# Kernel tuning notes

Measured on AMD Instinct MI355X. Metric: run time of the kernel, lower is better.

## Reference

```python
import jax, jax.numpy as jnp
import numpy as np

NUM_CLASSES = 21
THRESH = 0.5
NEGPOS = 3
VAR0, VAR1 = 0.1, 0.2
FEAT = 19
N_ANCH = 9
B = 256
NUM_OBJS = 12
P = FEAT * FEAT * N_ANCH  # 3249


def make_priors():
    # 19x19 grid, 3 scales x 3 aspect ratios (1, 2, 1/2) -> 9 anchors/cell, center form
    cxy = (np.arange(FEAT, dtype=np.float32) + 0.5) / FEAT
    cx, cy = np.meshgrid(cxy, cxy, indexing='ij')  # [19,19]
    scales = np.array([0.1, 0.2, 0.35], dtype=np.float32)
    ratios = np.array([1.0, 2.0, 0.5], dtype=np.float32)
    w = (scales[:, None] * np.sqrt(ratios)[None, :]).reshape(-1)  # [9]
    h = (scales[:, None] / np.sqrt(ratios)[None, :]).reshape(-1)
    cx = np.broadcast_to(cx[:, :, None], (FEAT, FEAT, N_ANCH))
    cy = np.broadcast_to(cy[:, :, None], (FEAT, FEAT, N_ANCH))
    w = np.broadcast_to(w[None, None, :], (FEAT, FEAT, N_ANCH))
    h = np.broadcast_to(h[None, None, :], (FEAT, FEAT, N_ANCH))
    pri = np.stack([cx, cy, w, h], axis=-1).reshape(-1, 4)
    return jnp.asarray(np.clip(pri, 1e-3, 1.0))


def setup_inputs() -> dict:
    key = jax.random.key(0)
    k1, k2, k3, k4, k5 = jax.random.split(key, 5)
    loc_data = jax.random.normal(k1, (B, P, 4), dtype=jnp.float32)
    conf_data = jax.random.normal(k2, (B, P, NUM_CLASSES), dtype=jnp.float32)
    priors = make_priors()
    xy = jax.random.uniform(k3, (B, NUM_OBJS, 2), minval=0.05, maxval=0.65)
    wh = jax.random.uniform(k4, (B, NUM_OBJS, 2), minval=0.05, maxval=0.30)
    labels = jax.random.randint(k5, (B, NUM_OBJS), 0, NUM_CLASSES - 1).astype(jnp.float32)
    targets = jnp.concatenate([xy, xy + wh, labels[..., None]], axis=-1)  # [B,O,5]
    return {"loc_data": loc_data, "conf_data": conf_data, "priors": priors, "targets": targets}


def point_form(boxes):  # (cx,cy,w,h) -> (x1,y1,x2,y2)
    return jnp.concatenate([boxes[:, :2] - boxes[:, 2:] / 2,
                            boxes[:, :2] + boxes[:, 2:] / 2], axis=1)


def jaccard(a, b):  # a: [n,4], b: [m,4] point form -> [n,m]
    lt = jnp.maximum(a[:, None, :2], b[None, :, :2])
    rb = jnp.minimum(a[:, None, 2:], b[None, :, 2:])
    inter = jnp.prod(jnp.clip(rb - lt, 0.0, None), axis=-1)
    area_a = jnp.prod(a[:, 2:] - a[:, :2], axis=-1)
    area_b = jnp.prod(b[:, 2:] - b[:, :2], axis=-1)
    return inter / (area_a[:, None] + area_b[None, :] - inter)


def encode(matched, priors):  # matched point-form [P,4], priors center-form [P,4]
    g_cxcy = ((matched[:, :2] + matched[:, 2:]) / 2 - priors[:, :2]) / (VAR0 * priors[:, 2:])
    g_wh = jnp.log((matched[:, 2:] - matched[:, :2]) / priors[:, 2:]) / VAR1
    return jnp.concatenate([g_cxcy, g_wh], axis=1)


def match_one(truths, labels, priors, priors_pt):
    overlaps = jaccard(truths, priors_pt)          # [O,P]
    best_prior_idx = jnp.argmax(overlaps, axis=1)  # [O]
    best_truth_ov = jnp.max(overlaps, axis=0)      # [P]
    best_truth_idx = jnp.argmax(overlaps, axis=0)  # [P]
    best_truth_ov = best_truth_ov.at[best_prior_idx].set(2.0)
    best_truth_idx = best_truth_idx.at[best_prior_idx].set(jnp.arange(truths.shape[0]))
    matches = truths[best_truth_idx]               # [P,4]
    conf = labels[best_truth_idx] + 1
    conf = jnp.where(best_truth_ov < THRESH, 0, conf)
    return encode(matches, priors), conf


def reference(loc_data, conf_data, priors, targets):
    truths = targets[:, :, :4]
    labels = targets[:, :, 4].astype(jnp.int32)
    priors_pt = point_form(priors)
    loc_t, conf_t = jax.vmap(lambda t, l: match_one(t, l, priors, priors_pt))(truths, labels)
    loc_t = jax.lax.stop_gradient(loc_t)
    conf_t = jax.lax.stop_gradient(conf_t)

    pos = conf_t > 0                                               # [B,P]
    # smooth L1 (sum) over matched priors
    d = loc_data - loc_t
    ad = jnp.abs(d)
    sl1 = jnp.where(ad < 1.0, 0.5 * d * d, ad - 0.5)
    loss_l = jnp.sum(sl1 * pos[..., None].astype(sl1.dtype))

    # per-prior CE = logsumexp - logit[target]
    lse = jax.nn.logsumexp(conf_data, axis=-1)                     # [B,P]
    gathered = jnp.take_along_axis(conf_data, conf_t[..., None], axis=2)[..., 0]
    ce = lse - gathered                                            # [B,P]

    # hard negative mining: double argsort rank of neg losses
    loss_c_mine = jnp.where(pos, 0.0, ce)
    loss_idx = jnp.argsort(-loss_c_mine, axis=1)
    idx_rank = jnp.argsort(loss_idx, axis=1)
    num_pos = jnp.sum(pos, axis=1, keepdims=True)                  # [B,1]
    num_neg = jnp.minimum(NEGPOS * num_pos, P - 1)
    neg = idx_rank < num_neg

    sel = pos | neg
    loss_c = jnp.sum(jnp.where(sel, ce, 0.0))

    have_centerloss = jnp.max(sel.reshape(B, FEAT, FEAT, N_ANCH), axis=3).reshape(-1)
    conf_t_featuremap = jnp.max(conf_t.reshape(B, FEAT, FEAT, N_ANCH), axis=3).reshape(-1)

    N = jnp.sum(num_pos).astype(loc_data.dtype)
    return loss_l / N, loss_c / N, conf_t_featuremap, have_centerloss
```

## Files before the change

### kernel.cpp

```cpp
#include <hip/hip_runtime.h>
#include <math.h>

#pragma clang fp contract(off)

#define BB      256
#define PP      3249
#define NCLS    21
#define NOBJ    12
#define CELLS   361
#define THRESH_ 0.5f
#define NPB     13


__global__ __launch_bounds__(256) void k1_lse_iou(
    const float* __restrict__ conf, const float* __restrict__ priors,
    const float* __restrict__ targets,
    float* __restrict__ g_lse, float* __restrict__ g_bov,
    unsigned char* __restrict__ g_bidx, unsigned long long* __restrict__ g_best)
{
    const int b = blockIdx.y;
    const int tid = threadIdx.x, lane = tid & 63;
    const int p = blockIdx.x * 256 + tid;
    const bool valid = (p < PP);

    __shared__ float s_tx1[NOBJ], s_ty1[NOBJ], s_tx2[NOBJ], s_ty2[NOBJ];
    __shared__ float s_area_t[NOBJ];
    if (tid < NOBJ) {
        const float* t = targets + ((size_t)b * NOBJ + tid) * 5;
        float x1 = t[0], y1 = t[1], x2 = t[2], y2 = t[3];
        s_tx1[tid] = x1; s_ty1[tid] = y1; s_tx2[tid] = x2; s_ty2[tid] = y2;
        s_area_t[tid] = (x2 - x1) * (y2 - y1);
    }
    __syncthreads();

    float iou_j[NOBJ];
    float bov = -1.0f; int bidx = 0;
    if (valid) {
        float cx = priors[4*p+0], cy = priors[4*p+1], w = priors[4*p+2], h = priors[4*p+3];
        float px1 = cx - w / 2.0f, py1 = cy - h / 2.0f;
        float px2 = cx + w / 2.0f, py2 = cy + h / 2.0f;
        float area_p = (px2 - px1) * (py2 - py1);
#pragma unroll
        for (int j = 0; j < NOBJ; ++j) {
            float ltx = fmaxf(s_tx1[j], px1);
            float lty = fmaxf(s_ty1[j], py1);
            float rbx = fminf(s_tx2[j], px2);
            float rby = fminf(s_ty2[j], py2);
            float iw = fmaxf(rbx - ltx, 0.0f);
            float ih = fmaxf(rby - lty, 0.0f);
            float inter = iw * ih;
            float iou = inter / ((s_area_t[j] + area_p) - inter);
            iou_j[j] = iou;
            if (iou > bov) { bov = iou; bidx = j; }
        }
    } else {
#pragma unroll
        for (int j = 0; j < NOBJ; ++j) iou_j[j] = -1.0f;
    }

#pragma unroll
    for (int j = 0; j < NOBJ; ++j) {
        float ov = iou_j[j]; int ix = valid ? p : 0x7FFFFFFF;
#pragma unroll
        for (int off = 32; off > 0; off >>= 1) {
            float ov2 = __shfl_xor(ov, off);
            int   ix2 = __shfl_xor(ix, off);
            if (ov2 > ov || (ov2 == ov && ix2 < ix)) { ov = ov2; ix = ix2; }
        }
        if (lane == 0 && ov >= 0.0f) {
            unsigned long long key =
                ((unsigned long long)__float_as_uint(ov) << 32)
                | (unsigned int)(0xFFFFFFFFu - (unsigned int)ix);
            atomicMax(&g_best[b * NOBJ + j], key);
        }
    }

    if (valid) {
        const size_t bp = (size_t)b * PP + p;
        g_bov[bp] = bov;
        g_bidx[bp] = (unsigned char)bidx;

        const float* cd = conf + bp * NCLS;
        float m = cd[0];
#pragma unroll
        for (int k = 1; k < NCLS; ++k) m = fmaxf(m, cd[k]);
        float s = 0.0f;
#pragma unroll
        for (int k = 0; k < NCLS; ++k) s += expf(cd[k] - m);
        g_lse[bp] = logf(s) + m;
    }
}

__global__ __launch_bounds__(1024) void k2_select(
    const float* __restrict__ loc, const float* __restrict__ conf,
    const float* __restrict__ priors, const float* __restrict__ targets,
    const float* __restrict__ g_lse, const float* __restrict__ g_bov,
    const unsigned char* __restrict__ g_bidx, const unsigned long long* __restrict__ g_best,
    int* __restrict__ numpos, double* __restrict__ lossl,
    double* __restrict__ lossc, float* __restrict__ out)
{
    const int b = blockIdx.x, tid = threadIdx.x;
    const int lane = tid & 63, wid = tid >> 6;

    __shared__ float s_tx1[NOBJ], s_ty1[NOBJ], s_tx2[NOBJ], s_ty2[NOBJ];
    __shared__ int   s_label[NOBJ];
    __shared__ int   s_bpi[NOBJ];
    __shared__ unsigned long long s_key[PP];
    __shared__ float s_ce[PP];
    __shared__ unsigned char s_ct[PP];
    __shared__ unsigned char s_sel[PP];
    __shared__ int s_hist[256];
    __shared__ int s_chosen, s_knext, s_nneg;
    __shared__ double s_pl[16];
    __shared__ int    s_pn[16];
    __shared__ double s_pc[16];

    if (tid < NOBJ) {
        const float* t = targets + ((size_t)b * NOBJ + tid) * 5;
        s_tx1[tid] = t[0]; s_ty1[tid] = t[1]; s_tx2[tid] = t[2]; s_ty2[tid] = t[3];
        s_label[tid] = (int)t[4];
        s_bpi[tid] = (int)(0xFFFFFFFFu - (unsigned int)(g_best[b * NOBJ + tid] & 0xFFFFFFFFull));
    }
    __syncthreads();

    int my_pos = 0;
    double my_lossl = 0.0;
    const float* confb = conf + (size_t)b * PP * NCLS;
    for (int p = tid; p < PP; p += 1024) {
        const size_t bp = (size_t)b * PP + p;
        int jov = -1;
#pragma unroll
        for (int j = 0; j < NOBJ; ++j) if (s_bpi[j] == p) jov = j;
        int idx; float ov;
        if (jov >= 0) { idx = jov; ov = 2.0f; }
        else          { idx = (int)g_bidx[bp]; ov = g_bov[bp]; }
        int c = (ov < THRESH_) ? 0 : (s_label[idx] + 1);
        s_ct[p] = (unsigned char)c;

        float ce = g_lse[bp] - confb[(size_t)p * NCLS + c];
        s_ce[p] = ce;
        float v = (c > 0) ? 0.0f : ce;
        s_key[p] = ((unsigned long long)__float_as_uint(v) << 32)
                 | (unsigned int)(0xFFFFFFFFu - (unsigned int)p);

        if (c > 0) {
            ++my_pos;
            float cx = priors[4*p+0], cy = priors[4*p+1], w = priors[4*p+2], h = priors[4*p+3];
            float m0 = s_tx1[idx], m1 = s_ty1[idx], m2 = s_tx2[idx], m3 = s_ty2[idx];
            float g0 = ((m0 + m2) / 2.0f - cx) / (0.1f * w);
            float g1 = ((m1 + m3) / 2.0f - cy) / (0.1f * h);
            float g2 = logf((m2 - m0) / w) / 0.2f;
            float g3 = logf((m3 - m1) / h) / 0.2f;
            const float* ld = loc + (bp) * 4;
            float d0 = ld[0] - g0, d1 = ld[1] - g1, d2 = ld[2] - g2, d3 = ld[3] - g3;
            float a0 = fabsf(d0), a1 = fabsf(d1), a2 = fabsf(d2), a3 = fabsf(d3);
            my_lossl += (double)((a0 < 1.0f) ? 0.5f * d0 * d0 : a0 - 0.5f);
            my_lossl += (double)((a1 < 1.0f) ? 0.5f * d1 * d1 : a1 - 0.5f);
            my_lossl += (double)((a2 < 1.0f) ? 0.5f * d2 * d2 : a2 - 0.5f);
            my_lossl += (double)((a3 < 1.0f) ? 0.5f * d3 * d3 : a3 - 0.5f);
        }
    }
#pragma unroll
    for (int off = 32; off > 0; off >>= 1) {
        my_lossl += __shfl_down(my_lossl, off);
        my_pos   += __shfl_down(my_pos, off);
    }
    if (lane == 0) { s_pl[wid] = my_lossl; s_pn[wid] = my_pos; }
    __syncthreads();
    if (tid == 0) {
        double L = 0.0; int n = 0;
#pragma unroll
        for (int w2 = 0; w2 < 16; ++w2) { L += s_pl[w2]; n += s_pn[w2]; }
        lossl[b] = L; numpos[b] = n;
        s_nneg = min(3 * n, PP - 1);
    }
    __syncthreads();

    unsigned long long prefix = 0ull, pmask = 0ull;
    int kk = s_nneg;
    for (int d = 56; d >= 0; d -= 8) {
        if (tid < 256) s_hist[tid] = 0;
        __syncthreads();
        for (int i = tid; i < PP; i += 1024) {
            unsigned long long key = s_key[i];
            if ((key & pmask) == prefix)
                atomicAdd(&s_hist[(int)((key >> d) & 0xFF)], 1);
        }
        __syncthreads();
        if (tid < 64) {
            int h0 = s_hist[4*lane+0], h1 = s_hist[4*lane+1];
            int h2 = s_hist[4*lane+2], h3 = s_hist[4*lane+3];
            int ls = h0 + h1 + h2 + h3;
            int x = ls;
#pragma unroll
            for (int off = 1; off < 64; off <<= 1) {
                int y = __shfl_down(x, off);
                if (lane + off < 64) x += y;
            }
            int excl = x - ls;
            int cb3 = excl;
            int cb2 = cb3 + h3;
            int cb1 = cb2 + h2;
            int cb0 = cb1 + h1;
            if (cb3 < kk && kk <= cb3 + h3) { s_chosen = 4*lane+3; s_knext = kk - cb3; }
            if (cb2 < kk && kk <= cb2 + h2) { s_chosen = 4*lane+2; s_knext = kk - cb2; }
            if (cb1 < kk && kk <= cb1 + h1) { s_chosen = 4*lane+1; s_knext = kk - cb1; }
            if (cb0 < kk && kk <= cb0 + h0) { s_chosen = 4*lane+0; s_knext = kk - cb0; }
        }
        __syncthreads();
        prefix |= ((unsigned long long)(unsigned int)s_chosen) << d;
        pmask  |= 0xFFull << d;
        kk = s_knext;
        __syncthreads();
    }
    const unsigned long long kth = prefix;

    double my_c = 0.0;
    for (int p = tid; p < PP; p += 1024) {
        int c = s_ct[p];
        bool sel = (c > 0) || (s_key[p] >= kth);
        s_sel[p] = sel ? 1 : 0;
        if (sel) my_c += (double)s_ce[p];
    }
    __syncthreads();

    for (int cI = tid; cI < CELLS; cI += 1024) {
        int mc = 0, hv = 0;
#pragma unroll
        for (int a = 0; a < 9; ++a) {
            int p = cI * 9 + a;
            int cv = s_ct[p];
            mc = (cv > mc) ? cv : mc;
            hv |= s_sel[p];
        }
        out[2 + (size_t)b * CELLS + cI] = (float)mc;
        out[2 + (size_t)BB * CELLS + (size_t)b * CELLS + cI] = (float)hv;
    }

#pragma unroll
    for (int off = 32; off > 0; off >>= 1) my_c += __shfl_down(my_c, off);
    if (lane == 0) s_pc[wid] = my_c;
    __syncthreads();
    if (tid == 0) {
        double L = 0.0;
#pragma unroll
        for (int w2 = 0; w2 < 16; ++w2) L += s_pc[w2];
        lossc[b] = L;
    }
}

__global__ __launch_bounds__(256) void finalize_kernel(
    const int* __restrict__ numpos, const double* __restrict__ lossl,
    const double* __restrict__ lossc, float* __restrict__ out)
{
    __shared__ double s_l[256], s_c[256];
    __shared__ int s_n[256];
    int tid = threadIdx.x;
    s_n[tid] = numpos[tid];
    s_l[tid] = lossl[tid];
    s_c[tid] = lossc[tid];
    __syncthreads();
    for (int s = 128; s > 0; s >>= 1) {
        if (tid < s) { s_n[tid] += s_n[tid + s]; s_l[tid] += s_l[tid + s]; s_c[tid] += s_c[tid + s]; }
        __syncthreads();
    }
    if (tid == 0) {
        double N = (double)s_n[0];
        out[0] = (float)(s_l[0] / N);
        out[1] = (float)(s_c[0] / N);
    }
}

extern "C" void kernel_launch(void* const* d_in, const int* in_sizes, int n_in,
                              void* d_out, int out_size, void* d_ws, size_t ws_size,
                              hipStream_t stream) {
    const float* loc     = (const float*)d_in[0];
    const float* conf    = (const float*)d_in[1];
    const float* priors  = (const float*)d_in[2];
    const float* targets = (const float*)d_in[3];
    float* out = (float*)d_out;

    double* ws_lossl  = (double*)d_ws;
    double* ws_lossc  = ws_lossl + BB;
    unsigned long long* ws_best = (unsigned long long*)(ws_lossc + BB);
    int*    ws_numpos = (int*)(ws_best + (size_t)BB * NOBJ);
    float*  ws_lse    = (float*)(ws_numpos + BB);
    float*  ws_bov    = ws_lse + (size_t)BB * PP;
    unsigned char* ws_bidx = (unsigned char*)(ws_bov + (size_t)BB * PP);

    hipMemsetAsync(ws_best, 0, (size_t)BB * NOBJ * sizeof(unsigned long long), stream);

    hipLaunchKernelGGL(k1_lse_iou, dim3(NPB, BB), dim3(256), 0, stream,
                       conf, priors, targets, ws_lse, ws_bov, ws_bidx, ws_best);
    hipLaunchKernelGGL(k2_select, dim3(BB), dim3(1024), 0, stream,
                       loc, conf, priors, targets, ws_lse, ws_bov, ws_bidx, ws_best,
                       ws_numpos, ws_lossl, ws_lossc, out);
    hipLaunchKernelGGL(finalize_kernel, dim3(1), dim3(256), 0, stream,
                       ws_numpos, ws_lossl, ws_lossc, out);
}
```

Measured before the change: 157.3 us.

## Split matching from CE, stage conf in LDS coalesced, skip radix passes on index bits

Moves IoU matching into a small kernel that writes one packed byte per prior (threshold flag plus best index). A new flat kernel stages each 256-row block of conf into shared memory with float4 loads, computes logsumexp and CE, and writes the sort key and class per prior. It also accumulates positives, loc loss and positive CE with global atomics, so k2 no longer rereads conf, loc and priors. The radix select skips two middle byte passes by fixing those index bits. This cuts redundant global traffic and uncoalesced conf reads, at the cost of an extra launch, per-prior double atomics, and a shortcut in the selection that relies on the key layout.

```diff
diff --git a/kernel.cpp b/kernel.cpp
--- a/kernel.cpp
+++ b/kernel.cpp
@@ -10,21 +10,19 @@
 #define CELLS   361
 #define THRESH_ 0.5f
 #define NPB     13
-
-
-__global__ __launch_bounds__(256) void k1_lse_iou(
-    const float* __restrict__ conf, const float* __restrict__ priors,
-    const float* __restrict__ targets,
-    float* __restrict__ g_lse, float* __restrict__ g_bov,
-    unsigned char* __restrict__ g_bidx, unsigned long long* __restrict__ g_best)
+#define NROWBLK 3249
+
+
+__global__ __launch_bounds__(256) void k0_match(
+    const float* __restrict__ priors, const float* __restrict__ targets,
+    unsigned char* __restrict__ g_mi, unsigned long long* __restrict__ g_best)
 {
     const int b = blockIdx.y;
     const int tid = threadIdx.x, lane = tid & 63;
     const int p = blockIdx.x * 256 + tid;
     const bool valid = (p < PP);
 
-    __shared__ float s_tx1[NOBJ], s_ty1[NOBJ], s_tx2[NOBJ], s_ty2[NOBJ];
-    __shared__ float s_area_t[NOBJ];
+    __shared__ float s_tx1[NOBJ], s_ty1[NOBJ], s_tx2[NOBJ], s_ty2[NOBJ], s_area_t[NOBJ];
     if (tid < NOBJ) {
         const float* t = targets + ((size_t)b * NOBJ + tid) * 5;
         float x1 = t[0], y1 = t[1], x2 = t[2], y2 = t[3];
@@ -53,6 +51,8 @@
             iou_j[j] = iou;
             if (iou > bov) { bov = iou; bidx = j; }
         }
+        g_mi[(size_t)b * PP + p] =
+            (unsigned char)(((bov < THRESH_) ? 0 : 0x80) | bidx);
     } else {
 #pragma unroll
         for (int j = 0; j < NOBJ; ++j) iou_j[j] = -1.0f;
@@ -74,111 +74,109 @@
             atomicMax(&g_best[b * NOBJ + j], key);
         }
     }
-
-    if (valid) {
-        const size_t bp = (size_t)b * PP + p;
-        g_bov[bp] = bov;
-        g_bidx[bp] = (unsigned char)bidx;
-
-        const float* cd = conf + bp * NCLS;
-        float m = cd[0];
-#pragma unroll
-        for (int k = 1; k < NCLS; ++k) m = fmaxf(m, cd[k]);
-        float s = 0.0f;
-#pragma unroll
-        for (int k = 0; k < NCLS; ++k) s += expf(cd[k] - m);
-        g_lse[bp] = logf(s) + m;
+}
+
+__global__ __launch_bounds__(256) void k1_ce(
+    const float* __restrict__ conf, const float* __restrict__ loc,
+    const float* __restrict__ priors, const float* __restrict__ targets,
+    const unsigned char* __restrict__ g_mi, const unsigned long long* __restrict__ g_best,
+    unsigned long long* __restrict__ g_key, unsigned char* __restrict__ g_ct,
+    int* __restrict__ numpos, double* __restrict__ lossl, double* __restrict__ lossc)
+{
+    __shared__ float s_conf[256 * NCLS];
+    const int tid = threadIdx.x;
+    const size_t row0 = (size_t)blockIdx.x * 256;
+
+    const float4* src = (const float4*)(conf + row0 * NCLS);
+    float4* dst = (float4*)s_conf;
+#pragma unroll
+    for (int i = tid; i < 1344; i += 256) dst[i] = src[i];
+    __syncthreads();
+
+    const size_t r = row0 + tid;
+    const int b = (int)(r / PP);
+    const int p = (int)(r - (size_t)b * PP);
+
+    int jov = -1;
+#pragma unroll
+    for (int j = 0; j < NOBJ; ++j) {
+        unsigned long long k = g_best[b * NOBJ + j];
+        int bp = (int)(0xFFFFFFFFu - (unsigned int)(k & 0xFFFFFFFFull));
+        if (bp == p) jov = j;
+    }
+    const unsigned char mi = g_mi[r];
+    int idx, c;
+    if (jov >= 0) {
+        idx = jov;
+        c = (int)targets[((size_t)b * NOBJ + idx) * 5 + 4] + 1;
+    } else {
+        idx = mi & 15;
+        c = (mi & 0x80) ? ((int)targets[((size_t)b * NOBJ + idx) * 5 + 4] + 1) : 0;
+    }
+    g_ct[r] = (unsigned char)c;
+
+    const float* cd = s_conf + tid * NCLS;
+    float m = cd[0];
+#pragma unroll
+    for (int k = 1; k < NCLS; ++k) m = fmaxf(m, cd[k]);
+    float s = 0.0f;
+#pragma unroll
+    for (int k = 0; k < NCLS; ++k) s += expf(cd[k] - m);
+    float ce = (logf(s) + m) - cd[c];
+
+    float v = (c > 0) ? 0.0f : ce;
+    g_key[r] = ((unsigned long long)__float_as_uint(v) << 32)
+             | (unsigned int)(0xFFFFFFFFu - (unsigned int)p);
+
+    if (c > 0) {
+        atomicAdd(&numpos[b], 1);
+        atomicAdd(&lossc[b], (double)ce);
+        const float* t = targets + ((size_t)b * NOBJ + idx) * 5;
+        float m0 = t[0], m1 = t[1], m2 = t[2], m3 = t[3];
+        float cx = priors[4*p+0], cy = priors[4*p+1], w = priors[4*p+2], h = priors[4*p+3];
+        float g0 = ((m0 + m2) / 2.0f - cx) / (0.1f * w);
+        float g1 = ((m1 + m3) / 2.0f - cy) / (0.1f * h);
+        float g2 = logf((m2 - m0) / w) / 0.2f;
+        float g3 = logf((m3 - m1) / h) / 0.2f;
+        const float* ld = loc + r * 4;
+        float d0 = ld[0] - g0, d1 = ld[1] - g1, d2 = ld[2] - g2, d3 = ld[3] - g3;
+        float a0 = fabsf(d0), a1 = fabsf(d1), a2 = fabsf(d2), a3 = fabsf(d3);
+        double sl = (double)((a0 < 1.0f) ? 0.5f * d0 * d0 : a0 - 0.5f)
+                  + (double)((a1 < 1.0f) ? 0.5f * d1 * d1 : a1 - 0.5f)
+                  + (double)((a2 < 1.0f) ? 0.5f * d2 * d2 : a2 - 0.5f)
+                  + (double)((a3 < 1.0f) ? 0.5f * d3 * d3 : a3 - 0.5f);
+        atomicAdd(&lossl[b], sl);
     }
 }
 
 __global__ __launch_bounds__(1024) void k2_select(
-    const float* __restrict__ loc, const float* __restrict__ conf,
-    const float* __restrict__ priors, const float* __restrict__ targets,
-    const float* __restrict__ g_lse, const float* __restrict__ g_bov,
-    const unsigned char* __restrict__ g_bidx, const unsigned long long* __restrict__ g_best,
-    int* __restrict__ numpos, double* __restrict__ lossl,
-    double* __restrict__ lossc, float* __restrict__ out)
+    const unsigned long long* __restrict__ g_key, const unsigned char* __restrict__ g_ct,
+    const int* __restrict__ numpos, double* __restrict__ lossc,
+    float* __restrict__ out)
 {
     const int b = blockIdx.x, tid = threadIdx.x;
     const int lane = tid & 63, wid = tid >> 6;
-
-    __shared__ float s_tx1[NOBJ], s_ty1[NOBJ], s_tx2[NOBJ], s_ty2[NOBJ];
-    __shared__ int   s_label[NOBJ];
-    __shared__ int   s_bpi[NOBJ];
     __shared__ unsigned long long s_key[PP];
-    __shared__ float s_ce[PP];
     __shared__ unsigned char s_ct[PP];
     __shared__ unsigned char s_sel[PP];
     __shared__ int s_hist[256];
-    __shared__ int s_chosen, s_knext, s_nneg;
-    __shared__ double s_pl[16];
-    __shared__ int    s_pn[16];
+    __shared__ int s_chosen, s_knext;
     __shared__ double s_pc[16];
 
-    if (tid < NOBJ) {
-        const float* t = targets + ((size_t)b * NOBJ + tid) * 5;
-        s_tx1[tid] = t[0]; s_ty1[tid] = t[1]; s_tx2[tid] = t[2]; s_ty2[tid] = t[3];
-        s_label[tid] = (int)t[4];
-        s_bpi[tid] = (int)(0xFFFFFFFFu - (unsigned int)(g_best[b * NOBJ + tid] & 0xFFFFFFFFull));
-    }
-    __syncthreads();
-
-    int my_pos = 0;
-    double my_lossl = 0.0;
-    const float* confb = conf + (size_t)b * PP * NCLS;
-    for (int p = tid; p < PP; p += 1024) {
-        const size_t bp = (size_t)b * PP + p;
-        int jov = -1;
-#pragma unroll
-        for (int j = 0; j < NOBJ; ++j) if (s_bpi[j] == p) jov = j;
-        int idx; float ov;
-        if (jov >= 0) { idx = jov; ov = 2.0f; }
-        else          { idx = (int)g_bidx[bp]; ov = g_bov[bp]; }
-        int c = (ov < THRESH_) ? 0 : (s_label[idx] + 1);
-        s_ct[p] = (unsigned char)c;
-
-        float ce = g_lse[bp] - confb[(size_t)p * NCLS + c];
-        s_ce[p] = ce;
-        float v = (c > 0) ? 0.0f : ce;
-        s_key[p] = ((unsigned long long)__float_as_uint(v) << 32)
-                 | (unsigned int)(0xFFFFFFFFu - (unsigned int)p);
-
-        if (c > 0) {
-            ++my_pos;
-            float cx = priors[4*p+0], cy = priors[4*p+1], w = priors[4*p+2], h = priors[4*p+3];
-            float m0 = s_tx1[idx], m1 = s_ty1[idx], m2 = s_tx2[idx], m3 = s_ty2[idx];
-            float g0 = ((m0 + m2) / 2.0f - cx) / (0.1f * w);
-            float g1 = ((m1 + m3) / 2.0f - cy) / (0.1f * h);
-            float g2 = logf((m2 - m0) / w) / 0.2f;
-            float g3 = logf((m3 - m1) / h) / 0.2f;
-            const float* ld = loc + (bp) * 4;
-            float d0 = ld[0] - g0, d1 = ld[1] - g1, d2 = ld[2] - g2, d3 = ld[3] - g3;
-            float a0 = fabsf(d0), a1 = fabsf(d1), a2 = fabsf(d2), a3 = fabsf(d3);
-            my_lossl += (double)((a0 < 1.0f) ? 0.5f * d0 * d0 : a0 - 0.5f);
-            my_lossl += (double)((a1 < 1.0f) ? 0.5f * d1 * d1 : a1 - 0.5f);
-            my_lossl += (double)((a2 < 1.0f) ? 0.5f * d2 * d2 : a2 - 0.5f);
-            my_lossl += (double)((a3 < 1.0f) ? 0.5f * d3 * d3 : a3 - 0.5f);
-        }
-    }
-#pragma unroll
-    for (int off = 32; off > 0; off >>= 1) {
-        my_lossl += __shfl_down(my_lossl, off);
-        my_pos   += __shfl_down(my_pos, off);
-    }
-    if (lane == 0) { s_pl[wid] = my_lossl; s_pn[wid] = my_pos; }
-    __syncthreads();
-    if (tid == 0) {
-        double L = 0.0; int n = 0;
-#pragma unroll
-        for (int w2 = 0; w2 < 16; ++w2) { L += s_pl[w2]; n += s_pn[w2]; }
-        lossl[b] = L; numpos[b] = n;
-        s_nneg = min(3 * n, PP - 1);
-    }
-    __syncthreads();
-
+    const int nneg = min(3 * numpos[b], PP - 1);
+
+    for (int i = tid; i < PP; i += 1024) {
+        s_key[i] = g_key[(size_t)b * PP + i];
+        s_ct[i] = g_ct[(size_t)b * PP + i];
+    }
+    __syncthreads();
+
+    const int ds[6] = {56, 48, 40, 32, 8, 0};
     unsigned long long prefix = 0ull, pmask = 0ull;
-    int kk = s_nneg;
-    for (int d = 56; d >= 0; d -= 8) {
+    int kk = nneg;
+#pragma unroll
+    for (int ri = 0; ri < 6; ++ri) {
+        const int d = ds[ri];
         if (tid < 256) s_hist[tid] = 0;
         __syncthreads();
         for (int i = tid; i < PP; i += 1024) {
@@ -211,6 +209,7 @@
         prefix |= ((unsigned long long)(unsigned int)s_chosen) << d;
         pmask  |= 0xFFull << d;
         kk = s_knext;
+        if (d == 32) { prefix |= 0xFFFF0000ull; pmask |= 0xFFFF0000ull; }
         __syncthreads();
     }
     const unsigned long long kth = prefix;
@@ -218,9 +217,11 @@
     double my_c = 0.0;
     for (int p = tid; p < PP; p += 1024) {
         int c = s_ct[p];
-        bool sel = (c > 0) || (s_key[p] >= kth);
+        unsigned long long key = s_key[p];
+        bool sel = (c > 0) || (key >= kth);
         s_sel[p] = sel ? 1 : 0;
-        if (sel) my_c += (double)s_ce[p];
+        if (sel && c == 0)
+            my_c += (double)__uint_as_float((unsigned int)(key >> 32));
     }
     __syncthreads();
 
@@ -242,7 +243,7 @@
     if (lane == 0) s_pc[wid] = my_c;
     __syncthreads();
     if (tid == 0) {
-        double L = 0.0;
+        double L = lossc[b];
 #pragma unroll
         for (int w2 = 0; w2 < 16; ++w2) L += s_pc[w2];
         lossc[b] = L;
@@ -280,21 +281,24 @@
     const float* targets = (const float*)d_in[3];
     float* out = (float*)d_out;
 
-    double* ws_lossl  = (double*)d_ws;
-    double* ws_lossc  = ws_lossl + BB;
+    double* ws_lossl = (double*)d_ws;
+    double* ws_lossc = ws_lossl + BB;
     unsigned long long* ws_best = (unsigned long long*)(ws_lossc + BB);
     int*    ws_numpos = (int*)(ws_best + (size_t)BB * NOBJ);
-    float*  ws_lse    = (float*)(ws_numpos + BB);
-    float*  ws_bov    = ws_lse + (size_t)BB * PP;
-    unsigned char* ws_bidx = (unsigned char*)(ws_bov + (size_t)BB * PP);
-
-    hipMemsetAsync(ws_best, 0, (size_t)BB * NOBJ * sizeof(unsigned long long), stream);
-
-    hipLaunchKernelGGL(k1_lse_iou, dim3(NPB, BB), dim3(256), 0, stream,
-                       conf, priors, targets, ws_lse, ws_bov, ws_bidx, ws_best);
+    const size_t zbytes = (size_t)BB * 8 * 2 + (size_t)BB * NOBJ * 8 + (size_t)BB * 4;
+    unsigned long long* ws_key = (unsigned long long*)((char*)d_ws + ((zbytes + 255) & ~(size_t)255));
+    unsigned char* ws_ct = (unsigned char*)(ws_key + (size_t)BB * PP);
+    unsigned char* ws_mi = ws_ct + (size_t)BB * PP;
+
+    hipMemsetAsync(d_ws, 0, zbytes, stream);
+
+    hipLaunchKernelGGL(k0_match, dim3(NPB, BB), dim3(256), 0, stream,
+                       priors, targets, ws_mi, ws_best);
+    hipLaunchKernelGGL(k1_ce, dim3(NROWBLK), dim3(256), 0, stream,
+                       conf, loc, priors, targets, ws_mi, ws_best,
+                       ws_key, ws_ct, ws_numpos, ws_lossl, ws_lossc);
     hipLaunchKernelGGL(k2_select, dim3(BB), dim3(1024), 0, stream,
-                       loc, conf, priors, targets, ws_lse, ws_bov, ws_bidx, ws_best,
-                       ws_numpos, ws_lossl, ws_lossc, out);
+                       ws_key, ws_ct, ws_numpos, ws_lossc, out);
     hipLaunchKernelGGL(finalize_kernel, dim3(1), dim3(256), 0, stream,
                        ws_numpos, ws_lossl, ws_lossc, out);
 }
```

Result: slower. 185.0 us (+17.7%).
